# Optimization experiments

Measured on AMD Instinct MI355X. Metric: run time of the kernel, lower is better.

## Reference

```python
import jax, jax.numpy as jnp
import numpy as np

N, E = 50000, 300000
IN_DIM, CODE_DIM = 1024, 768
HID, HEADS, DH = 256, 4, 64
NUM_REL = 5
CODE_WEIGHT = 1.0


def setup_inputs() -> dict:
    key = jax.random.key(0)
    ks = jax.random.split(key, 24)
    p = lambda k, shape: jax.random.normal(k, shape, dtype=jnp.float32) * 0.05
    return {
        "x": jax.random.normal(ks[0], (N, IN_DIM), dtype=jnp.float32),
        "edge_index": jax.random.randint(ks[1], (2, E), 0, N, dtype=jnp.int64),
        "edge_type": jax.random.randint(ks[2], (E,), 0, NUM_REL, dtype=jnp.int64),
        "edge_weight": jax.random.uniform(ks[3], (E,), dtype=jnp.float32),
        "rel_emb": p(ks[4], (NUM_REL, HID)),
        "W_in": p(ks[5], (HID, IN_DIM)),
        "b_in": jnp.zeros((HID,), jnp.float32),
        "W1": p(ks[6], (HEADS * DH, HID)),
        "a1_src": p(ks[7], (HEADS, DH)),
        "a1_dst": p(ks[8], (HEADS, DH)),
        "b1": jnp.zeros((HEADS * DH,), jnp.float32),
        "W2": p(ks[9], (HEADS * DH, HID)),
        "a2_src": p(ks[10], (HEADS, DH)),
        "a2_dst": p(ks[11], (HEADS, DH)),
        "b2": jnp.zeros((HEADS * DH,), jnp.float32),
        "ln1_g": jnp.ones((HID,), jnp.float32),
        "ln1_b": jnp.zeros((HID,), jnp.float32),
        "ln2_g": jnp.ones((HID,), jnp.float32),
        "ln2_b": jnp.zeros((HID,), jnp.float32),
        "W_out": p(ks[12], (1, HID)),
        "b_out": jnp.zeros((1,), jnp.float32),
    }


def _layer_norm(x, g, b, eps=1e-5):
    m = x.mean(-1, keepdims=True)
    v = ((x - m) ** 2).mean(-1, keepdims=True)
    return (x - m) * jax.lax.rsqrt(v + eps) * g + b


def _gat_conv(h, s_all, d_all, W, a_src, a_dst, bias):
    # PyG GATConv (concat=True, negative_slope=0.2), self-loops already in s_all/d_all
    xh = (h @ W.T).reshape(N, HEADS, DH)                      # [N,H,DH]
    al_s = (xh * a_src).sum(-1)                                # [N,H]
    al_d = (xh * a_dst).sum(-1)                                # [N,H]
    e = jax.nn.leaky_relu(al_s[s_all] + al_d[d_all], 0.2)      # [E+N,H]
    mx = jax.ops.segment_max(e, d_all, num_segments=N)         # segment softmax over dst
    ex = jnp.exp(e - mx[d_all])
    den = jax.ops.segment_sum(ex, d_all, num_segments=N)
    alpha = ex / (den[d_all] + 1e-16)
    out = jax.ops.segment_sum(xh[s_all] * alpha[:, :, None], d_all, num_segments=N)
    return out.reshape(N, HEADS * DH) + bias


def reference(x, edge_index, edge_type, edge_weight, rel_emb, W_in, b_in,
              W1, a1_src, a1_dst, b1, W2, a2_src, a2_dst, b2,
              ln1_g, ln1_b, ln2_g, ln2_b, W_out, b_out):
    # split (code_at_front=True), standardize numeric, l2-normalize code
    x_code = x[:, :CODE_DIM]
    x_num = x[:, CODE_DIM:]
    m = x_num.mean(0, keepdims=True)
    s = jnp.maximum(x_num.std(0, ddof=1, keepdims=True), 1e-6)
    x_num = (x_num - m) / s
    nrm = jnp.maximum(jnp.linalg.norm(x_code, axis=1, keepdims=True), 1e-12)
    x_code = x_code / nrm
    xin = jnp.concatenate([x_num, CODE_WEIGHT * x_code], axis=-1)

    h = jax.nn.relu(xin @ W_in.T + b_in)                       # [N,HID]

    src, dst = edge_index[0], edge_index[1]
    rel = rel_emb[edge_type] * edge_weight[:, None]            # [E,HID]
    msg = h[src] + rel
    h = h.at[dst].add(msg)                                     # index_add

    loop = jnp.arange(N, dtype=src.dtype)                      # GATConv add_self_loops
    s_all = jnp.concatenate([src, loop])
    d_all = jnp.concatenate([dst, loop])

    h1 = _gat_conv(h, s_all, d_all, W1, a1_src, a1_dst, b1)
    h = _layer_norm(h1 + h, ln1_g, ln1_b)
    h2 = _gat_conv(h, s_all, d_all, W2, a2_src, a2_dst, b2)
    h = _layer_norm(h2 + h, ln2_g, ln2_b)
    return (h @ W_out.T + b_out).squeeze(-1)                   # [N]
```

## Files before the change

kernel.cpp:

```cpp
#include <hip/hip_runtime.h>
#include <math.h>

constexpr int NN   = 50000;
constexpr int EE   = 300000;
constexpr int IND  = 1024;
constexpr int CODE = 768;
constexpr int HID  = 256;

typedef __bf16 bf16_t;
typedef bf16_t bf16x4 __attribute__((ext_vector_type(4)));
typedef bf16_t bf16x8 __attribute__((ext_vector_type(8)));
typedef float  f32x4  __attribute__((ext_vector_type(4)));

__device__ __forceinline__ f32x4 mfma16(bf16x8 a, bf16x8 b, f32x4 c) {
    return __builtin_amdgcn_mfma_f32_16x16x32_bf16(a, b, c, 0, 0, 0);
}

#define GLOAD_LDS16(gp, lp) __builtin_amdgcn_global_load_lds(                         \
    (__attribute__((address_space(1))) void*)(gp),                                    \
    (__attribute__((address_space(3))) void*)(lp), 16, 0, 0)

__device__ __forceinline__ f32x4 ld_bf4(const bf16_t* p) {
    bf16x4 v = *(const bf16x4*)p;
    f32x4 r;
    r[0] = (float)v[0]; r[1] = (float)v[1]; r[2] = (float)v[2]; r[3] = (float)v[3];
    return r;
}

__global__ void colstats_kernel(const float* __restrict__ x, float* __restrict__ sums) {
    int col = threadIdx.x;
    float s = 0.f, s2 = 0.f;
    for (int row = blockIdx.x; row < NN; row += gridDim.x) {
        float v = x[(size_t)row * IND + CODE + col];
        s += v; s2 += v * v;
    }
    atomicAdd(&sums[col], s);
    atomicAdd(&sums[256 + col], s2);
}

__global__ void xin_kernel(const float* __restrict__ x, const float* __restrict__ sums,
                           bf16_t* __restrict__ xin)
{
    int lane = threadIdx.x & 63, wid = threadIdx.x >> 6;
    int row  = blockIdx.x * 4 + wid;
    if (row >= NN) return;
    const f32x4* x4 = (const f32x4*)(x + (size_t)row * IND);
    f32x4 v[4];
    #pragma unroll
    for (int i = 0; i < 4; i++) v[i] = x4[lane + 64 * i];
    float s = 0.f;
    #pragma unroll
    for (int i = 0; i < 3; i++)
        s += v[i][0] * v[i][0] + v[i][1] * v[i][1] + v[i][2] * v[i][2] + v[i][3] * v[i][3];
    #pragma unroll
    for (int off = 32; off; off >>= 1) s += __shfl_xor(s, off);
    float inr = 1.f / fmaxf(sqrtf(s), 1e-12f);

    bf16_t* xr = xin + (size_t)row * IND;
    #pragma unroll
    for (int i = 0; i < 3; i++) {
        bf16x4 o;
        #pragma unroll
        for (int q = 0; q < 4; q++) o[q] = (bf16_t)(v[i][q] * inr);
        *(bf16x4*)(xr + 256 + 4 * (lane + 64 * i)) = o;
    }
    {
        bf16x4 o;
        #pragma unroll
        for (int q = 0; q < 4; q++) {
            int j = 4 * lane + q;
            float mean = sums[j] / (float)NN;
            float var  = (sums[256 + j] - (float)NN * mean * mean) / (float)(NN - 1);
            float invstd = 1.f / fmaxf(sqrtf(fmaxf(var, 0.f)), 1e-6f);
            o[q] = (bf16_t)((v[3][q] - mean) * invstd);
        }
        *(bf16x4*)(xr + 4 * lane) = o;
    }
}

__global__ void prep_all_kernel(const float* __restrict__ W_in, const float* __restrict__ W1,
                                const float* __restrict__ W2, bf16_t* __restrict__ Wmh,
                                bf16_t* __restrict__ Wh1, bf16_t* __restrict__ Wh2)
{
    int b = blockIdx.x, t = threadIdx.x;
    if (b < 1024) {
        size_t i = (size_t)b * 256 + t;
        Wmh[i] = (bf16_t)W_in[i];
    } else if (b < 1280) {
        size_t i = (size_t)(b - 1024) * 256 + t;
        Wh1[i] = (bf16_t)W1[i];
    } else {
        size_t i = (size_t)(b - 1280) * 256 + t;
        Wh2[i] = (bf16_t)W2[i];
    }
}


__device__ __forceinline__ void stage_b(const bf16_t* __restrict__ src, int n0, int ldk,
                                        int maxrow, int k0, bf16_t* buf, int tid) {
    int w = tid >> 6, l = tid & 63;
    #pragma unroll
    for (int i = 0; i < 2; i++) {
        int gbase = w * 128 + i * 64;
        bf16_t* dst = buf + gbase * 8;
        int g = gbase + l;
        int col = g >> 2, p = g & 3;
        int gs = p ^ ((col >> 1) & 3);
        int row = n0 + col;
        if (row > maxrow) row = maxrow;
        const bf16_t* gp = src + (size_t)row * ldk + k0 + gs * 8;
        GLOAD_LDS16(gp, dst);
    }
}

template<int MODE, int K, int FATTN>
__global__ __launch_bounds__(256) void gemm_mfma_kernel(
    const bf16_t* __restrict__ A16, const bf16_t* __restrict__ Bh,
    const float* __restrict__ bin, const float* __restrict__ a_src,
    const float* __restrict__ a_dst, float* __restrict__ out,
    bf16_t* __restrict__ xhb, float* __restrict__ al_s, float* __restrict__ al_d)
{
    __shared__ bf16_t Asb[2][128 * 32];
    __shared__ bf16_t Bhs[2][128 * 32];
    constexpr int NT = K / 32;

    int tid  = threadIdx.x;
    int lane = tid & 63;
    int w    = tid >> 6;
    int wr   = w >> 1, wc = w & 1;
    int r0   = blockIdx.x * 128, n0 = blockIdx.y * 128;

    f32x4 acc[4][4];
    #pragma unroll
    for (int i = 0; i < 4; i++)
        #pragma unroll
        for (int j = 0; j < 4; j++) acc[i][j] = (f32x4)0.f;

    int kc = lane >> 4, fr = lane & 15;

    stage_b(A16, r0, K, NN - 1, 0, Asb[0], tid);
    stage_b(Bh, n0, K, 255, 0, Bhs[0], tid);
    __syncthreads();

    for (int t = 0; t < NT; ++t) {
        int buf = t & 1;
        if (t + 1 < NT) {
            stage_b(A16, r0, K, NN - 1, (t + 1) * 32, Asb[buf ^ 1], tid);
            stage_b(Bh, n0, K, 255, (t + 1) * 32, Bhs[buf ^ 1], tid);
        }
        const bf16_t* Ab = Asb[buf];
        const bf16_t* Hb = Bhs[buf];
        bf16x8 ahi[4];
        #pragma unroll
        for (int mf = 0; mf < 4; mf++) {
            int r  = wr * 64 + mf * 16 + fr;
            int pr = kc ^ ((r >> 1) & 3);
            ahi[mf] = *(const bf16x8*)&Ab[r * 32 + pr * 8];
        }
        #pragma unroll
        for (int nf = 0; nf < 4; nf++) {
            int c  = wc * 64 + nf * 16 + fr;
            int pr = kc ^ ((c >> 1) & 3);
            bf16x8 bhi = *(const bf16x8*)&Hb[c * 32 + pr * 8];
            #pragma unroll
            for (int mf = 0; mf < 4; mf++)
                acc[mf][nf] = mfma16(ahi[mf], bhi, acc[mf][nf]);
        }
        __syncthreads();
    }

    int head = blockIdx.y * 2 + wc;
    float asv[4], adv[4];
    if (FATTN) {
        #pragma unroll
        for (int nf = 0; nf < 4; nf++) {
            asv[nf] = a_src[head * 64 + nf * 16 + fr];
            adv[nf] = a_dst[head * 64 + nf * 16 + fr];
        }
    }
    #pragma unroll
    for (int mf = 0; mf < 4; mf++) {
        #pragma unroll
        for (int j = 0; j < 4; j++) {
            int row = r0 + wr * 64 + mf * 16 + kc * 4 + j;
            bool ok = row < NN;
            float s = 0.f, d = 0.f;
            #pragma unroll
            for (int nf = 0; nf < 4; nf++) {
                int col = n0 + wc * 64 + nf * 16 + fr;
                float v = acc[mf][nf][j];
                if (MODE == 1) {
                    v = fmaxf(v + bin[col], 0.f);
                    if (ok) out[(size_t)row * HID + col] = v;
                }
                if (FATTN) {
                    s += v * asv[nf]; d += v * adv[nf];
                    if (ok) xhb[(size_t)row * HID + col] = (bf16_t)v;
                }
            }
            if (FATTN) {
                #pragma unroll
                for (int off = 1; off < 16; off <<= 1) {
                    s += __shfl_xor(s, off);
                    d += __shfl_xor(d, off);
                }
                if (ok && fr == 0) {
                    al_s[row * 4 + head] = s;
                    al_d[row * 4 + head] = d;
                }
            }
        }
    }
}

__global__ void deg_kernel(const int* __restrict__ ei, int* __restrict__ deg) {
    int e = blockIdx.x * 256 + threadIdx.x;
    if (e < EE) atomicAdd(&deg[ei[EE + e]], 1);
}

constexpr int SCB = 1024;
constexpr int SCN = (NN + SCB - 1) / SCB;

__global__ void scan_pass1(const int* __restrict__ deg, int* __restrict__ bsum) {
    int b = blockIdx.x, t = threadIdx.x;
    int base = b * SCB + t * 4;
    int s = 0;
    #pragma unroll
    for (int i = 0; i < 4; i++) { int idx = base + i; if (idx < NN) s += deg[idx]; }
    #pragma unroll
    for (int off = 32; off; off >>= 1) s += __shfl_xor(s, off);
    __shared__ int ps[4];
    if ((t & 63) == 0) ps[t >> 6] = s;
    __syncthreads();
    if (t == 0) bsum[b] = ps[0] + ps[1] + ps[2] + ps[3];
}

__global__ void scan_pass2(int* __restrict__ bsum) {
    int t = threadIdx.x;
    int orig = (t < SCN) ? bsum[t] : 0;
    int v = orig;
    for (int off = 1; off < 64; off <<= 1) {
        int u = __shfl_up(v, off);
        if (t >= off) v += u;
    }
    if (t < SCN) bsum[t] = v - orig;
}

__global__ void scan_pass3(const int* __restrict__ deg, const int* __restrict__ boffs,
                           int* __restrict__ row_ptr, int* __restrict__ cursor) {
    int b = blockIdx.x, t = threadIdx.x;
    int base = b * SCB + t * 4;
    int d[4]; int tot = 0;
    #pragma unroll
    for (int i = 0; i < 4; i++) { int idx = base + i; d[i] = (idx < NN) ? deg[idx] : 0; tot += d[i]; }
    int v = tot;
    for (int off = 1; off < 64; off <<= 1) {
        int u = __shfl_up(v, off);
        if ((t & 63) >= off) v += u;
    }
    __shared__ int wsum[4];
    if ((t & 63) == 63) wsum[t >> 6] = v;
    __syncthreads();
    int woff = 0;
    for (int j = 0; j < (t >> 6); j++) woff += wsum[j];
    int run = boffs[b] + woff + v - tot;
    #pragma unroll
    for (int i = 0; i < 4; i++) {
        int idx = base + i;
        if (idx < NN) {
            cursor[idx] = run;
            run += d[i];
            row_ptr[idx + 1] = run;
        }
    }
    if (b == 0 && t == 0) row_ptr[0] = 0;
}

__global__ void fill_kernel(const int* __restrict__ ei, const int* __restrict__ etype,
                            const float* __restrict__ ew, int* __restrict__ cursor,
                            int* __restrict__ csr_src, int* __restrict__ csr_t,
                            float* __restrict__ csr_w) {
    int e = blockIdx.x * 256 + threadIdx.x;
    if (e >= EE) return;
    int dst = ei[EE + e];
    int pos = atomicAdd(&cursor[dst], 1);
    csr_src[pos] = ei[e];
    csr_t[pos]   = etype[e];
    csr_w[pos]   = ew[e];
}

__global__ void relagg_kernel(const float* __restrict__ h, const int* __restrict__ row_ptr,
                              const int* __restrict__ csr_src, const int* __restrict__ csr_t,
                              const float* __restrict__ csr_w,
                              const float* __restrict__ rel_emb, float* __restrict__ out,
                              bf16_t* __restrict__ out16)
{
    int lane = threadIdx.x & 63, wid = threadIdx.x >> 6;
    int node = blockIdx.x * 4 + wid;
    if (node >= NN) return;
    int c0 = lane * 4;
    f32x4 acc = *(const f32x4*)(h + (size_t)node * HID + c0);
    float wsum[5] = {0.f, 0.f, 0.f, 0.f, 0.f};
    int beg = row_ptr[node], end = row_ptr[node + 1];
    for (int k = beg; k < end; k += 8) {
        int s[8], tt[8]; float ww[8], vm[8];
        #pragma unroll
        for (int j = 0; j < 8; j++) {
            int kk = k + j;
            bool valid = kk < end;
            kk = valid ? kk : (end - 1);
            s[j]  = csr_src[kk];
            tt[j] = csr_t[kk];
            ww[j] = valid ? csr_w[kk] : 0.f;
            vm[j] = valid ? 1.f : 0.f;
        }
        f32x4 xv[8];
        #pragma unroll
        for (int j = 0; j < 8; j++) xv[j] = *(const f32x4*)(h + (size_t)s[j] * HID + c0);
        #pragma unroll
        for (int j = 0; j < 8; j++) {
            acc += vm[j] * xv[j];
            #pragma unroll
            for (int r = 0; r < 5; r++) wsum[r] += (tt[j] == r) ? ww[j] : 0.f;
        }
    }
    #pragma unroll
    for (int r = 0; r < 5; r++)
        acc += wsum[r] * *(const f32x4*)(rel_emb + r * HID + c0);
    *(f32x4*)(out + (size_t)node * HID + c0) = acc;
    bf16x4 a16;
    #pragma unroll
    for (int i = 0; i < 4; i++) a16[i] = (bf16_t)acc[i];
    *(bf16x4*)(out16 + (size_t)node * HID + c0) = a16;
}

template<int FINAL>
__global__ void gat_kernel(const bf16_t* __restrict__ xhb, const float* __restrict__ al_s,
                           const float* __restrict__ al_d, const int* __restrict__ row_ptr,
                           const int* __restrict__ csr_src, const float* __restrict__ h_res,
                           const float* __restrict__ bias, const float* __restrict__ ln_g,
                           const float* __restrict__ ln_b, float* __restrict__ out,
                           bf16_t* __restrict__ out16,
                           const float* __restrict__ W_out, const float* __restrict__ b_out,
                           float* __restrict__ final_out)
{
    int lane = threadIdx.x & 63, wid = threadIdx.x >> 6;
    int node = blockIdx.x * 4 + wid;
    if (node >= NN) return;
    int hh = lane >> 4;
    int c0 = lane * 4;

    float ald = al_d[node * 4 + hh];
    float m, den;
    f32x4 acc;

    {
        float als = al_s[node * 4 + hh];
        float e = als + ald;
        e = (e >= 0.f) ? e : 0.2f * e;
        m = e; den = 1.f;
        acc = ld_bf4(xhb + (size_t)node * HID + c0);
    }

    int beg = row_ptr[node], end = row_ptr[node + 1];
    for (int k = beg; k < end; k += 8) {
        int s[8]; float als[8];
        #pragma unroll
        for (int j = 0; j < 8; j++) {
            int kk = k + j;
            bool valid = kk < end;
            s[j] = csr_src[valid ? kk : (end - 1)];
            als[j] = valid ? 0.f : -INFINITY;
        }
        #pragma unroll
        for (int j = 0; j < 8; j++)
            if (als[j] == 0.f) als[j] = al_s[s[j] * 4 + hh];
        f32x4 xv[8];
        #pragma unroll
        for (int j = 0; j < 8; j++) xv[j] = ld_bf4(xhb + (size_t)s[j] * HID + c0);
        #pragma unroll
        for (int j = 0; j < 8; j++) {
            float e = als[j] + ald;
            e = (e >= 0.f) ? e : 0.2f * e;
            float mn  = fmaxf(m, e);
            float f   = __expf(m - mn);
            float wgt = __expf(e - mn);
            m   = mn;
            den = den * f + wgt;
            acc = acc * f + wgt * xv[j];
        }
    }

    f32x4 bia = *(const f32x4*)(bias + c0);
    f32x4 res = *(const f32x4*)(h_res + (size_t)node * HID + c0);
    f32x4 z;
    float rd = 1.f / (den + 1e-16f);
    #pragma unroll
    for (int i = 0; i < 4; i++) z[i] = acc[i] * rd + bia[i] + res[i];

    float s = z[0] + z[1] + z[2] + z[3];
    #pragma unroll
    for (int off = 32; off; off >>= 1) s += __shfl_xor(s, off);
    float mean = s * (1.f / 256.f);
    float vp = 0.f;
    #pragma unroll
    for (int i = 0; i < 4; i++) { float d2 = z[i] - mean; vp += d2 * d2; }
    #pragma unroll
    for (int off = 32; off; off >>= 1) vp += __shfl_xor(vp, off);
    float rstd = rsqrtf(vp * (1.f / 256.f) + 1e-5f);

    f32x4 g = *(const f32x4*)(ln_g + c0);
    f32x4 bb = *(const f32x4*)(ln_b + c0);
    if (FINAL) {
        f32x4 wo = *(const f32x4*)(W_out + c0);
        float dot = 0.f;
        #pragma unroll
        for (int i = 0; i < 4; i++)
            dot += ((z[i] - mean) * rstd * g[i] + bb[i]) * wo[i];
        #pragma unroll
        for (int off = 32; off; off >>= 1) dot += __shfl_xor(dot, off);
        if (lane == 0) final_out[node] = dot + b_out[0];
    } else {
        f32x4 o;
        bf16x4 o16;
        #pragma unroll
        for (int i = 0; i < 4; i++) {
            o[i] = (z[i] - mean) * rstd * g[i] + bb[i];
            o16[i] = (bf16_t)o[i];
        }
        *(f32x4*)(out + (size_t)node * HID + c0) = o;
        *(bf16x4*)(out16 + (size_t)node * HID + c0) = o16;
    }
}

extern "C" void kernel_launch(void* const* d_in, const int* in_sizes, int n_in,
                              void* d_out, int out_size, void* d_ws, size_t ws_size,
                              hipStream_t stream) {
    const float* x       = (const float*)d_in[0];
    const int*   ei      = (const int*)d_in[1];
    const int*   etype   = (const int*)d_in[2];
    const float* ew      = (const float*)d_in[3];
    const float* rel_emb = (const float*)d_in[4];
    const float* W_in    = (const float*)d_in[5];
    const float* b_in    = (const float*)d_in[6];
    const float* W1      = (const float*)d_in[7];
    const float* a1s     = (const float*)d_in[8];
    const float* a1d     = (const float*)d_in[9];
    const float* b1      = (const float*)d_in[10];
    const float* W2      = (const float*)d_in[11];
    const float* a2s     = (const float*)d_in[12];
    const float* a2d     = (const float*)d_in[13];
    const float* b2      = (const float*)d_in[14];
    const float* ln1g    = (const float*)d_in[15];
    const float* ln1b    = (const float*)d_in[16];
    const float* ln2g    = (const float*)d_in[17];
    const float* ln2b    = (const float*)d_in[18];
    const float* W_out   = (const float*)d_in[19];
    const float* b_out   = (const float*)d_in[20];
    float* out = (float*)d_out;

    char* ws = (char*)d_ws;
    auto alloc = [&](size_t bytes) {
        void* p = (void*)ws;
        ws += (bytes + 255) & ~(size_t)255;
        return p;
    };
    float*  bufA     = (float*)alloc((size_t)NN * HID * 4);
    float*  bufB     = (float*)alloc((size_t)NN * HID * 4);
    bf16_t* xin16    = (bf16_t*)alloc((size_t)NN * IND * 2);
    bf16_t* xhb      = (bf16_t*)alloc((size_t)NN * HID * 2);
    bf16_t* gin16    = (bf16_t*)alloc((size_t)NN * HID * 2);
    bf16_t* wmh      = (bf16_t*)alloc((size_t)HID * IND * 2);
    bf16_t* w1h      = (bf16_t*)alloc((size_t)HID * HID * 2);
    bf16_t* w2h      = (bf16_t*)alloc((size_t)HID * HID * 2);
    float*  stats_s  = (float*)alloc(512 * 4);
    float*  al_s     = (float*)alloc((size_t)NN * 4 * 4);
    float*  al_d     = (float*)alloc((size_t)NN * 4 * 4);
    int*    deg      = (int*)alloc((size_t)NN * 4);
    int*    row_ptr  = (int*)alloc((size_t)(NN + 1) * 4);
    int*    cursor   = (int*)alloc((size_t)NN * 4);
    int*    csr_src  = (int*)alloc((size_t)EE * 4);
    int*    csr_t    = (int*)alloc((size_t)EE * 4);
    float*  csr_w    = (float*)alloc((size_t)EE * 4);
    int*    bsum     = (int*)alloc(64 * 4);

    hipMemsetAsync(stats_s, 0, 512 * 4, stream);
    hipMemsetAsync(deg, 0, (size_t)NN * 4, stream);

    colstats_kernel<<<1024, 256, 0, stream>>>(x, stats_s);
    xin_kernel<<<(NN + 3) / 4, 256, 0, stream>>>(x, stats_s, xin16);
    prep_all_kernel<<<1536, 256, 0, stream>>>(W_in, W1, W2, wmh, w1h, w2h);

    deg_kernel<<<(EE + 255) / 256, 256, 0, stream>>>(ei, deg);
    scan_pass1<<<SCN, 256, 0, stream>>>(deg, bsum);
    scan_pass2<<<1, 64, 0, stream>>>(bsum);
    scan_pass3<<<SCN, 256, 0, stream>>>(deg, bsum, row_ptr, cursor);
    fill_kernel<<<(EE + 255) / 256, 256, 0, stream>>>(ei, etype, ew, cursor,
                                                      csr_src, csr_t, csr_w);

    dim3 g1((NN + 127) / 128, 2);

    gemm_mfma_kernel<1, 1024, 0><<<g1, 256, 0, stream>>>(
        xin16, wmh, b_in, nullptr, nullptr, bufA, nullptr, nullptr, nullptr);

    int nodeBlocks = (NN + 3) / 4;

    relagg_kernel<<<nodeBlocks, 256, 0, stream>>>(bufA, row_ptr, csr_src, csr_t, csr_w,
                                                  rel_emb, bufB, gin16);

    gemm_mfma_kernel<0, 256, 1><<<g1, 256, 0, stream>>>(
        gin16, w1h, nullptr, a1s, a1d, nullptr, xhb, al_s, al_d);
    gat_kernel<0><<<nodeBlocks, 256, 0, stream>>>(xhb, al_s, al_d, row_ptr, csr_src,
                                                  bufB, b1, ln1g, ln1b, bufA, gin16,
                                                  nullptr, nullptr, nullptr);

    gemm_mfma_kernel<0, 256, 1><<<g1, 256, 0, stream>>>(
        gin16, w2h, nullptr, a2s, a2d, nullptr, xhb, al_s, al_d);
    gat_kernel<1><<<nodeBlocks, 256, 0, stream>>>(xhb, al_s, al_d, row_ptr, csr_src,
                                                  bufA, b2, ln2g, ln2b, nullptr, nullptr,
                                                  W_out, b_out, out);
}
```

Measured before the change: 417.1 us.

## Remap GEMM block order, gather bf16 features in relagg, merge scan passes

The GEMM grid becomes 1D and is remapped so that groups of 8 row tiles run both column halves next to each other, which is meant to improve L2 reuse of the A rows. The first GEMM now also writes a bf16 copy of h, and the relational aggregation gathers neighbour rows from that copy instead of fp32 to halve gather traffic, at the cost of an extra write and reduced precision. The first two scan passes are merged into one single-block kernel to save a launch.

```diff
diff --git a/kernel.cpp b/kernel.cpp
--- a/kernel.cpp
+++ b/kernel.cpp
@@ -6,6 +6,10 @@
 constexpr int IND  = 1024;
 constexpr int CODE = 768;
 constexpr int HID  = 256;
+
+constexpr int NRT   = (NN + 127) / 128;
+constexpr int NFULL = (NRT / 8) * 16;
+constexpr int NTAIL = NRT % 8;
 
 typedef __bf16 bf16_t;
 typedef bf16_t bf16x4 __attribute__((ext_vector_type(4)));
@@ -128,7 +132,11 @@
     int lane = tid & 63;
     int w    = tid >> 6;
     int wr   = w >> 1, wc = w & 1;
-    int r0   = blockIdx.x * 128, n0 = blockIdx.y * 128;
+
+    int bid = blockIdx.x, rt, ch;
+    if (bid < NFULL) { rt = (bid >> 4) * 8 + (bid & 7); ch = (bid >> 3) & 1; }
+    else { int i = bid - NFULL; rt = (NRT / 8) * 8 + i % NTAIL; ch = i / NTAIL; }
+    int r0 = rt * 128, n0 = ch * 128;
 
     f32x4 acc[4][4];
     #pragma unroll
@@ -169,7 +177,7 @@
         __syncthreads();
     }
 
-    int head = blockIdx.y * 2 + wc;
+    int head = ch * 2 + wc;
     float asv[4], adv[4];
     if (FATTN) {
         #pragma unroll
@@ -191,7 +199,10 @@
                 float v = acc[mf][nf][j];
                 if (MODE == 1) {
                     v = fmaxf(v + bin[col], 0.f);
-                    if (ok) out[(size_t)row * HID + col] = v;
+                    if (ok) {
+                        out[(size_t)row * HID + col] = v;
+                        xhb[(size_t)row * HID + col] = (bf16_t)v;
+                    }
                 }
                 if (FATTN) {
                     s += v * asv[nf]; d += v * adv[nf];
@@ -221,29 +232,24 @@
 constexpr int SCB = 1024;
 constexpr int SCN = (NN + SCB - 1) / SCB;
 
-__global__ void scan_pass1(const int* __restrict__ deg, int* __restrict__ bsum) {
-    int b = blockIdx.x, t = threadIdx.x;
-    int base = b * SCB + t * 4;
-    int s = 0;
-    #pragma unroll
-    for (int i = 0; i < 4; i++) { int idx = base + i; if (idx < NN) s += deg[idx]; }
-    #pragma unroll
-    for (int off = 32; off; off >>= 1) s += __shfl_xor(s, off);
-    __shared__ int ps[4];
-    if ((t & 63) == 0) ps[t >> 6] = s;
+__global__ void scan12_kernel(const int* __restrict__ deg, int* __restrict__ bsum) {
+    __shared__ int sh[SCN];
+    int tid = threadIdx.x, w = tid >> 6, lane = tid & 63;
+    for (int b = w; b < SCN; b += 16) {
+        int s = 0;
+        for (int i = lane; i < SCB; i += 64) {
+            int idx = b * SCB + i;
+            if (idx < NN) s += deg[idx];
+        }
+        #pragma unroll
+        for (int off = 32; off; off >>= 1) s += __shfl_xor(s, off);
+        if (lane == 0) sh[b] = s;
+    }
     __syncthreads();
-    if (t == 0) bsum[b] = ps[0] + ps[1] + ps[2] + ps[3];
-}
-
-__global__ void scan_pass2(int* __restrict__ bsum) {
-    int t = threadIdx.x;
-    int orig = (t < SCN) ? bsum[t] : 0;
-    int v = orig;
-    for (int off = 1; off < 64; off <<= 1) {
-        int u = __shfl_up(v, off);
-        if (t >= off) v += u;
-    }
-    if (t < SCN) bsum[t] = v - orig;
+    if (tid == 0) {
+        int run = 0;
+        for (int b = 0; b < SCN; b++) { int v = sh[b]; bsum[b] = run; run += v; }
+    }
 }
 
 __global__ void scan_pass3(const int* __restrict__ deg, const int* __restrict__ boffs,
@@ -289,7 +295,8 @@
     csr_w[pos]   = ew[e];
 }
 
-__global__ void relagg_kernel(const float* __restrict__ h, const int* __restrict__ row_ptr,
+__global__ void relagg_kernel(const float* __restrict__ h, const bf16_t* __restrict__ h16,
+                              const int* __restrict__ row_ptr,
                               const int* __restrict__ csr_src, const int* __restrict__ csr_t,
                               const float* __restrict__ csr_w,
                               const float* __restrict__ rel_emb, float* __restrict__ out,
@@ -316,7 +323,7 @@
         }
         f32x4 xv[8];
         #pragma unroll
-        for (int j = 0; j < 8; j++) xv[j] = *(const f32x4*)(h + (size_t)s[j] * HID + c0);
+        for (int j = 0; j < 8; j++) xv[j] = ld_bf4(h16 + (size_t)s[j] * HID + c0);
         #pragma unroll
         for (int j = 0; j < 8; j++) {
             acc += vm[j] * xv[j];
@@ -470,6 +477,7 @@
     bf16_t* xin16    = (bf16_t*)alloc((size_t)NN * IND * 2);
     bf16_t* xhb      = (bf16_t*)alloc((size_t)NN * HID * 2);
     bf16_t* gin16    = (bf16_t*)alloc((size_t)NN * HID * 2);
+    bf16_t* hb16     = (bf16_t*)alloc((size_t)NN * HID * 2);
     bf16_t* wmh      = (bf16_t*)alloc((size_t)HID * IND * 2);
     bf16_t* w1h      = (bf16_t*)alloc((size_t)HID * HID * 2);
     bf16_t* w2h      = (bf16_t*)alloc((size_t)HID * HID * 2);
@@ -492,29 +500,28 @@
     prep_all_kernel<<<1536, 256, 0, stream>>>(W_in, W1, W2, wmh, w1h, w2h);
 
     deg_kernel<<<(EE + 255) / 256, 256, 0, stream>>>(ei, deg);
-    scan_pass1<<<SCN, 256, 0, stream>>>(deg, bsum);
-    scan_pass2<<<1, 64, 0, stream>>>(bsum);
+    scan12_kernel<<<1, 1024, 0, stream>>>(deg, bsum);
     scan_pass3<<<SCN, 256, 0, stream>>>(deg, bsum, row_ptr, cursor);
     fill_kernel<<<(EE + 255) / 256, 256, 0, stream>>>(ei, etype, ew, cursor,
                                                       csr_src, csr_t, csr_w);
 
-    dim3 g1((NN + 127) / 128, 2);
-
-    gemm_mfma_kernel<1, 1024, 0><<<g1, 256, 0, stream>>>(
-        xin16, wmh, b_in, nullptr, nullptr, bufA, nullptr, nullptr, nullptr);
+    int gemmGrid = NFULL + 2 * NTAIL;
+
+    gemm_mfma_kernel<1, 1024, 0><<<gemmGrid, 256, 0, stream>>>(
+        xin16, wmh, b_in, nullptr, nullptr, bufA, hb16, nullptr, nullptr);
 
     int nodeBlocks = (NN + 3) / 4;
 
-    relagg_kernel<<<nodeBlocks, 256, 0, stream>>>(bufA, row_ptr, csr_src, csr_t, csr_w,
-                                                  rel_emb, bufB, gin16);
-
-    gemm_mfma_kernel<0, 256, 1><<<g1, 256, 0, stream>>>(
+    relagg_kernel<<<nodeBlocks, 256, 0, stream>>>(bufA, hb16, row_ptr, csr_src, csr_t,
+                                                  csr_w, rel_emb, bufB, gin16);
+
+    gemm_mfma_kernel<0, 256, 1><<<gemmGrid, 256, 0, stream>>>(
         gin16, w1h, nullptr, a1s, a1d, nullptr, xhb, al_s, al_d);
     gat_kernel<0><<<nodeBlocks, 256, 0, stream>>>(xhb, al_s, al_d, row_ptr, csr_src,
                                                   bufB, b1, ln1g, ln1b, bufA, gin16,
                                                   nullptr, nullptr, nullptr);
 
-    gemm_mfma_kernel<0, 256, 1><<<g1, 256, 0, stream>>>(
+    gemm_mfma_kernel<0, 256, 1><<<gemmGrid, 256, 0, stream>>>(
         gin16, w2h, nullptr, a2s, a2d, nullptr, xhb, al_s, al_d);
     gat_kernel<1><<<nodeBlocks, 256, 0, stream>>>(xhb, al_s, al_d, row_ptr, csr_src,
                                                   bufA, b2, ln2g, ln2b, nullptr, nullptr,
```

Measured after the change: 424.3 us. No clear change (+1.7%).
